# Performance work log

Hardware: AMD Instinct MI355X
Metric: run time of the kernel (lower is better)

The kernel has to match this reference:

```python
import jax, jax.numpy as jnp
import numpy as np

B, L, H = 32, 1024, 384


def setup_inputs() -> dict:
    key = jax.random.key(0)
    k1, k2 = jax.random.split(key)
    encoder_hidden_states = jax.random.normal(k1, (B, L, H), dtype=jnp.float32)
    durations_gt = jax.random.randint(k2, (B, L), 0, 8, dtype=jnp.int32)
    return {"encoder_hidden_states": encoder_hidden_states, "durations_gt": durations_gt}


def reference(encoder_hidden_states, durations_gt):
    # cumulative end-frame of each phoneme: [B, L]
    cum = jnp.cumsum(durations_gt, axis=1)
    total = cum[:, -1]                      # [B] expanded length per batch item
    T = int(jnp.max(total))                 # max expanded length (data-dependent)
    t = jnp.arange(T, dtype=cum.dtype)      # [T] output frame positions
    # source phoneme index for each output frame: number of cum entries <= t
    idx = jax.vmap(lambda c: jnp.searchsorted(c, t, side="right"))(cum)  # [B, T]
    idx = jnp.minimum(idx, L - 1)
    mask = (t[None, :] < total[:, None]).astype(jnp.float32)             # [B, T]
    # gather hidden states and zero out the padded tail
    out = jnp.take_along_axis(encoder_hidden_states, idx[:, :, None], axis=1)
    out = out * mask[:, :, None]
    return out, mask
```

## Files before the change

### kernel.cpp

```cpp
#include <hip/hip_runtime.h>

#define BB 32
#define LL 1024
#define HH 384
#define H4 (HH / 4)
#define TT 64
#define NT 256
#define NW (NT / 64)
#define WPT (TT * H4 / NT)

typedef float f4 __attribute__((ext_vector_type(4)));

__global__ __launch_bounds__(NT) void lenreg_kernel(
    const float* __restrict__ ehs,
    const int* __restrict__ dur,
    float* __restrict__ out,
    float* __restrict__ mask,
    int T)
{
    __shared__ int scum[LL];
    __shared__ int wsum[NW];
    __shared__ int sidx[TT];

    const int tid  = threadIdx.x;
    const int lane = tid & 63;
    const int wid  = tid >> 6;
    const int b    = blockIdx.y;
    const int t0   = blockIdx.x * TT;

    int4 d = ((const int4*)(dur + (size_t)b * LL))[tid];
    const int p0 = d.x;
    const int p1 = p0 + d.y;
    const int p2 = p1 + d.z;
    const int p3 = p2 + d.w;

    int v = p3;
    #pragma unroll
    for (int off = 1; off < 64; off <<= 1) {
        const int n = __shfl_up(v, off, 64);
        if (lane >= off) v += n;
    }
    if (lane == 63) wsum[wid] = v;
    __syncthreads();

    int woff = 0, total = 0;
    #pragma unroll
    for (int w = 0; w < NW; ++w) {
        const int s = wsum[w];
        woff  += (w < wid) ? s : 0;
        total += s;
    }

    const int excl = woff + v - p3;
    scum[4 * tid + 0] = excl + p0;
    scum[4 * tid + 1] = excl + p1;
    scum[4 * tid + 2] = excl + p2;
    scum[4 * tid + 3] = excl + p3;
    __syncthreads();

    if (tid < TT) {
        const int t = t0 + tid;
        int pos = 0;
        #pragma unroll
        for (int step = LL / 2; step > 0; step >>= 1) {
            if (scum[pos + step - 1] <= t) pos += step;
        }
        sidx[tid] = (pos < LL - 1) ? pos : (LL - 1);
        if (t < T) mask[(size_t)b * T + t] = (t < total) ? 1.0f : 0.0f;
    }
    __syncthreads();

    const f4* __restrict__ src = (const f4*)(ehs + (size_t)b * LL * HH);
    f4* __restrict__ ob = (f4*)out + ((size_t)b * T + t0) * (size_t)H4;

    const int tlim = (T < total) ? T : total;
    if (t0 + TT <= tlim) {
        int idxr[WPT];
        #pragma unroll
        for (int i = 0; i < WPT; ++i) {
            idxr[i] = sidx[(tid + i * NT) / H4];
        }
        #pragma unroll
        for (int i = 0; i < WPT; ++i) {
            const int w  = tid + i * NT;
            const int tl = w / H4;
            const int vv = w - tl * H4;
            const f4 val = src[(size_t)idxr[i] * H4 + vv];
            __builtin_nontemporal_store(val, &ob[w]);
        }
    } else {
        const int tend = (T < t0 + TT) ? T : (t0 + TT);
        const int wmax = (tend > t0) ? (tend - t0) * H4 : 0;
        const f4 zero4 = (f4){0.f, 0.f, 0.f, 0.f};
        for (int w = tid; w < wmax; w += NT) {
            const int tl = w / H4;
            const int vv = w - tl * H4;
            const int t  = t0 + tl;
            f4 val = zero4;
            if (t < total) val = src[(size_t)sidx[tl] * H4 + vv];
            __builtin_nontemporal_store(val, &ob[w]);
        }
    }
}

extern "C" void kernel_launch(void* const* d_in, const int* in_sizes, int n_in,
                              void* d_out, int out_size, void* d_ws, size_t ws_size,
                              hipStream_t stream) {
    const float* ehs = (const float*)d_in[0];
    const int*   dur = (const int*)d_in[1];

    const int T = out_size / (BB * (HH + 1));

    float* out  = (float*)d_out;
    float* mask = (float*)d_out + (size_t)BB * T * HH;

    dim3 grid((T + TT - 1) / TT, BB);
    dim3 block(NT);
    lenreg_kernel<<<grid, block, 0, stream>>>(ehs, dur, out, mask, T);
}
```

Baseline: 227.6 us.

## Split each batch row into fixed slabs of frames to amortize the prefix scan

The grid becomes a fixed 32 blocks per batch row instead of one block per 64 output frames. Each block now handles a contiguous slab of about T/32 frames, so the per-block 1024-entry prefix scan over durations is repeated far fewer times. The separate full-tile and tail paths are merged into one unrolled loop that uses a -1 index as the zero-padding sentinel. In exchange there are fewer blocks and so less parallelism for latency hiding, and the fixed shared index buffer breaks if a slab ever exceeds 256 frames.

```diff
diff --git a/kernel.cpp b/kernel.cpp
--- a/kernel.cpp
+++ b/kernel.cpp
@@ -4,10 +4,10 @@
 #define LL 1024
 #define HH 384
 #define H4 (HH / 4)
-#define TT 64
 #define NT 256
 #define NW (NT / 64)
-#define WPT (TT * H4 / NT)
+#define NB 32
+#define SMAX 256
 
 typedef float f4 __attribute__((ext_vector_type(4)));
 
@@ -20,13 +20,18 @@
 {
     __shared__ int scum[LL];
     __shared__ int wsum[NW];
-    __shared__ int sidx[TT];
+    __shared__ int sidx[SMAX];
 
     const int tid  = threadIdx.x;
     const int lane = tid & 63;
     const int wid  = tid >> 6;
     const int b    = blockIdx.y;
-    const int t0   = blockIdx.x * TT;
+
+    const int slab = (T + NB - 1) / NB;
+    const int ts   = blockIdx.x * slab;
+    const int te   = (ts + slab < T) ? (ts + slab) : T;
+    if (ts >= te) return;
+    const int n    = te - ts;
 
     int4 d = ((const int4*)(dur + (size_t)b * LL))[tid];
     const int p0 = d.x;
@@ -37,8 +42,8 @@
     int v = p3;
     #pragma unroll
     for (int off = 1; off < 64; off <<= 1) {
-        const int n = __shfl_up(v, off, 64);
-        if (lane >= off) v += n;
+        const int nn = __shfl_up(v, off, 64);
+        if (lane >= off) v += nn;
     }
     if (lane == 63) wsum[wid] = v;
     __syncthreads();
@@ -58,48 +63,32 @@
     scum[4 * tid + 3] = excl + p3;
     __syncthreads();
 
-    if (tid < TT) {
-        const int t = t0 + tid;
+    if (tid < n) {
+        const int t = ts + tid;
         int pos = 0;
         #pragma unroll
         for (int step = LL / 2; step > 0; step >>= 1) {
             if (scum[pos + step - 1] <= t) pos += step;
         }
-        sidx[tid] = (pos < LL - 1) ? pos : (LL - 1);
-        if (t < T) mask[(size_t)b * T + t] = (t < total) ? 1.0f : 0.0f;
+        pos = (pos < LL - 1) ? pos : (LL - 1);
+        sidx[tid] = (t < total) ? pos : -1;
+        mask[(size_t)b * T + t] = (t < total) ? 1.0f : 0.0f;
     }
     __syncthreads();
 
     const f4* __restrict__ src = (const f4*)(ehs + (size_t)b * LL * HH);
-    f4* __restrict__ ob = (f4*)out + ((size_t)b * T + t0) * (size_t)H4;
+    f4* __restrict__ ob = (f4*)out + ((size_t)b * T + ts) * (size_t)H4;
+    const int wmax = n * H4;
+    const f4 zero4 = (f4){0.f, 0.f, 0.f, 0.f};
 
-    const int tlim = (T < total) ? T : total;
-    if (t0 + TT <= tlim) {
-        int idxr[WPT];
-        #pragma unroll
-        for (int i = 0; i < WPT; ++i) {
-            idxr[i] = sidx[(tid + i * NT) / H4];
-        }
-        #pragma unroll
-        for (int i = 0; i < WPT; ++i) {
-            const int w  = tid + i * NT;
-            const int tl = w / H4;
-            const int vv = w - tl * H4;
-            const f4 val = src[(size_t)idxr[i] * H4 + vv];
-            __builtin_nontemporal_store(val, &ob[w]);
-        }
-    } else {
-        const int tend = (T < t0 + TT) ? T : (t0 + TT);
-        const int wmax = (tend > t0) ? (tend - t0) * H4 : 0;
-        const f4 zero4 = (f4){0.f, 0.f, 0.f, 0.f};
-        for (int w = tid; w < wmax; w += NT) {
-            const int tl = w / H4;
-            const int vv = w - tl * H4;
-            const int t  = t0 + tl;
-            f4 val = zero4;
-            if (t < total) val = src[(size_t)sidx[tl] * H4 + vv];
-            __builtin_nontemporal_store(val, &ob[w]);
-        }
+    #pragma unroll 4
+    for (int w = tid; w < wmax; w += NT) {
+        const int tl  = w / H4;
+        const int vv  = w - tl * H4;
+        const int idx = sidx[tl];
+        f4 val = zero4;
+        if (idx >= 0) val = src[(size_t)idx * H4 + vv];
+        __builtin_nontemporal_store(val, &ob[w]);
     }
 }
 
@@ -114,7 +103,7 @@
     float* out  = (float*)d_out;
     float* mask = (float*)d_out + (size_t)BB * T * HH;
 
-    dim3 grid((T + TT - 1) / TT, BB);
+    dim3 grid(NB, BB);
     dim3 block(NT);
     lenreg_kernel<<<grid, block, 0, stream>>>(ehs, dur, out, mask, T);
 }
```

After: 233.5 us. 1.03x slower.
